# Kernel optimization log

Hardware: AMD Instinct MI355X
Metric: run time of the kernel (lower is better)

The kernel has to match this reference:

```python
import jax, jax.numpy as jnp
import numpy as np

NUM_HEADS = 16
LN_EPS = 1e-05


def setup_inputs() -> dict:
    key = jax.random.key(0)
    ks = jax.random.split(key, 10)
    B, S, H = 2, 2048, 1024
    s = 1.0 / np.sqrt(H)
    return {
        "hidden_states": jax.random.normal(ks[0], (B, S, H), dtype=jnp.float32),
        "Wq": jax.random.normal(ks[1], (H, H), dtype=jnp.float32) * s,
        "bq": jax.random.normal(ks[2], (H,), dtype=jnp.float32) * 0.02,
        "Wk": jax.random.normal(ks[3], (H, H), dtype=jnp.float32) * s,
        "bk": jax.random.normal(ks[4], (H,), dtype=jnp.float32) * 0.02,
        "Wv": jax.random.normal(ks[5], (H, H), dtype=jnp.float32) * s,
        "bv": jax.random.normal(ks[6], (H,), dtype=jnp.float32) * 0.02,
        "Wd": jax.random.normal(ks[7], (H, H), dtype=jnp.float32) * s,
        "bd": jax.random.normal(ks[8], (H,), dtype=jnp.float32) * 0.02,
        "ln_gamma": jnp.ones((H,), dtype=jnp.float32),
        "ln_beta": jnp.zeros((H,), dtype=jnp.float32),
    }


def reference(hidden_states, Wq, bq, Wk, bk, Wv, bv, Wd, bd, ln_gamma, ln_beta):
    B, S, H = hidden_states.shape
    nh = NUM_HEADS
    hd = H // nh

    # QKV projections (torch Linear: x @ W.T + b), split heads -> [B, nh, S, hd]
    def proj(W, b):
        y = jnp.einsum('bsh,oh->bso', hidden_states, W) + b
        return y.reshape(B, S, nh, hd).transpose(0, 2, 1, 3)

    q = proj(Wq, bq)
    k = proj(Wk, bk)
    v = proj(Wv, bv)

    # scaled dot-product attention: [B, nh, S, S]
    scores = jnp.einsum('bhqd,bhkd->bhqk', q, k) / jnp.sqrt(jnp.float32(hd))
    probs = jax.nn.softmax(scores, axis=-1)
    ctx = jnp.einsum('bhqk,bhkd->bhqd', probs, v)  # [B, nh, S, hd]
    ctx = ctx.transpose(0, 2, 1, 3).reshape(B, S, H)

    # output dense + residual + LayerNorm
    attn_out = jnp.einsum('bsh,oh->bso', ctx, Wd) + bd
    x = attn_out + hidden_states
    mu = jnp.mean(x, axis=-1, keepdims=True)
    var = jnp.mean(jnp.square(x - mu), axis=-1, keepdims=True)
    return (x - mu) * jax.lax.rsqrt(var + LN_EPS) * ln_gamma + ln_beta
```

## Files before the change

kernel.cpp:

```cpp
#include <hip/hip_runtime.h>

constexpr int kH    = 1024;
constexpr int kSEQ  = 2048;
constexpr int kBATCH= 2;
constexpr int kNH   = 16;
constexpr int kHD   = 64;
constexpr int kM    = 4096;

typedef _Float16 h8  __attribute__((ext_vector_type(8)));
typedef _Float16 h4  __attribute__((ext_vector_type(4)));
typedef float   f32x4 __attribute__((ext_vector_type(4)));

static __device__ __forceinline__ f32x4 mfma16(h8 a, h8 b, f32x4 c) {
  return __builtin_amdgcn_mfma_f32_16x16x32_f16(a, b, c, 0, 0, 0);
}

static __device__ __forceinline__ void gll16(const _Float16* g, _Float16* l) {
  __builtin_amdgcn_global_load_lds(
      (const __attribute__((address_space(1))) void*)g,
      (__attribute__((address_space(3))) void*)l, 16, 0, 0);
}

#define QSCALE 0.18033688011112042f
#define C0INIT (-5.770780163555854f)

__global__ __launch_bounds__(256) void cvt_all(
    const float* __restrict__ X,  const float* __restrict__ Wq,
    const float* __restrict__ Wk, const float* __restrict__ Wv,
    const float* __restrict__ Wd,
    _Float16* __restrict__ Xh,  _Float16* __restrict__ Wqh,
    _Float16* __restrict__ Wkh, _Float16* __restrict__ Wvh,
    _Float16* __restrict__ Wdh)
{
  int i = blockIdx.x * 256 + threadIdx.x;
  const float* src; _Float16* dst; int off;
  if (i < (kM * kH) / 4) {
    src = X; dst = Xh; off = i;
  } else {
    int j = i - (kM * kH) / 4;
    int w = j >> 18;
    off = j & 262143;
    src = (w == 0) ? Wq : (w == 1) ? Wk : (w == 2) ? Wv : Wd;
    dst = (w == 0) ? Wqh : (w == 1) ? Wkh : (w == 2) ? Wvh : Wdh;
  }
  float4 v = reinterpret_cast<const float4*>(src)[off];
  h4 o;
  o[0] = (_Float16)v.x; o[1] = (_Float16)v.y;
  o[2] = (_Float16)v.z; o[3] = (_Float16)v.w;
  reinterpret_cast<h4*>(dst)[off] = o;
}

__global__ __launch_bounds__(256, 2) void qkv_gemm(
    const _Float16* __restrict__ Xh,
    const _Float16* __restrict__ Wq, const _Float16* __restrict__ Wk,
    const _Float16* __restrict__ Wv,
    const float* __restrict__ bq, const float* __restrict__ bk,
    const float* __restrict__ bv,
    _Float16* __restrict__ Qo, _Float16* __restrict__ Ko, _Float16* __restrict__ Vo)
{
  const int proj = blockIdx.z;
  const _Float16* W   = (proj == 0) ? Wq : ((proj == 1) ? Wk : Wv);
  const float*    bias= (proj == 0) ? bq : ((proj == 1) ? bk : bv);
  _Float16*       Out = (proj == 0) ? Qo : ((proj == 1) ? Ko : Vo);

  const int m0 = blockIdx.y * 128, n0 = blockIdx.x * 128;
  __shared__ __align__(16) _Float16 As[2][128 * 32];
  __shared__ __align__(16) _Float16 Bs[2][128 * 32];

  const int tid  = threadIdx.x;
  const int wave = tid >> 6, lane = tid & 63, quad = lane >> 4, l16 = lane & 15;
  const int mw = (wave & 1) * 64, nw = (wave >> 1) * 64;

  f32x4 acc[4][4] = {};
  const int grow = wave * 32 + (lane >> 2);
  const int gcol = (lane & 3) * 8;
  const _Float16* Ag = Xh + (size_t)(m0 + grow) * kH + gcol;
  const _Float16* Bg = W  + (size_t)(n0 + grow) * kH + gcol;

  {
    gll16(Ag,            &As[0][wave * 1024]);
    gll16(Ag + 16 * kH,  &As[0][wave * 1024 + 512]);
    gll16(Bg,            &Bs[0][wave * 1024]);
    gll16(Bg + 16 * kH,  &Bs[0][wave * 1024 + 512]);
  }

  for (int k = 0; k < 32; ++k) {
    const int cur = k & 1;
    __syncthreads();
    if (k < 31) {
      const int k0 = (k + 1) * 32, nb = cur ^ 1;
      gll16(Ag + k0,           &As[nb][wave * 1024]);
      gll16(Ag + 16 * kH + k0, &As[nb][wave * 1024 + 512]);
      gll16(Bg + k0,           &Bs[nb][wave * 1024]);
      gll16(Bg + 16 * kH + k0, &Bs[nb][wave * 1024 + 512]);
    }
    h8 af[4], bf[4];
    #pragma unroll
    for (int mi = 0; mi < 4; ++mi)
      af[mi] = *reinterpret_cast<const h8*>(&As[cur][(mw + mi * 16 + l16) * 32 + quad * 8]);
    #pragma unroll
    for (int ni = 0; ni < 4; ++ni)
      bf[ni] = *reinterpret_cast<const h8*>(&Bs[cur][(nw + ni * 16 + l16) * 32 + quad * 8]);
    #pragma unroll
    for (int mi = 0; mi < 4; ++mi)
      #pragma unroll
      for (int ni = 0; ni < 4; ++ni)
        acc[mi][ni] = mfma16(af[mi], bf[ni], acc[mi][ni]);
  }

  #pragma unroll
  for (int mi = 0; mi < 4; ++mi)
  #pragma unroll
  for (int ni = 0; ni < 4; ++ni) {
    const int ng = n0 + nw + ni * 16 + l16;
    const float bv_ = bias[ng];
    const int hh = ng >> 6, dd = ng & 63;
    #pragma unroll
    for (int r = 0; r < 4; ++r) {
      const int mg = m0 + mw + mi * 16 + quad * 4 + r;
      float val = acc[mi][ni][r] + bv_;
      if (proj == 0) val *= QSCALE;
      const int bb = mg >> 11, srow = mg & 2047;
      Out[(((size_t)(bb * kNH + hh) * kSEQ) + srow) * kHD + dd] = (_Float16)val;
    }
  }
}

__global__ __launch_bounds__(256) void vtrans(const _Float16* __restrict__ V,
                                              _Float16* __restrict__ Vt)
{
  const int st = blockIdx.x;
  const int bh = blockIdx.y;
  __shared__ __align__(16) _Float16 Lt[64][72];
  const int t = threadIdx.x, r = t >> 2, c = (t & 3) * 16;
  const _Float16* src = V + (size_t)bh * kSEQ * kHD + (size_t)(st * 64 + r) * kHD + c;
  h8 p0 = *reinterpret_cast<const h8*>(src);
  h8 p1 = *reinterpret_cast<const h8*>(src + 8);
  #pragma unroll
  for (int e = 0; e < 8; ++e) Lt[c + e][r] = p0[e];
  #pragma unroll
  for (int e = 0; e < 8; ++e) Lt[c + 8 + e][r] = p1[e];
  __syncthreads();
  _Float16* dst = Vt + (size_t)bh * kHD * kSEQ + (size_t)r * kSEQ + st * 64 + c;
  *reinterpret_cast<h8*>(dst)     = *reinterpret_cast<const h8*>(&Lt[r][c]);
  *reinterpret_cast<h8*>(dst + 8) = *reinterpret_cast<const h8*>(&Lt[r][c + 8]);
}

__global__ __launch_bounds__(256, 3) void attn_kernel(
    const _Float16* __restrict__ Q, const _Float16* __restrict__ K,
    const _Float16* __restrict__ Vt, _Float16* __restrict__ Ctx)
{
  const int qt = blockIdx.x, bh = blockIdx.y;
  const int tid = threadIdx.x;
  const int wave = tid >> 6, lane = tid & 63, quad = lane >> 4, l16 = lane & 15;
  const int sw = l16 & 7;

  __shared__ __align__(16) _Float16 Kl[2][64 * 64];
  __shared__ __align__(16) _Float16 Vl[2][64 * 64];
  __shared__ __align__(16) _Float16 Pl[4][32 * 64];

  const _Float16* Qb = Q  + (size_t)bh * kSEQ * kHD;
  const _Float16* Kb = K  + (size_t)bh * kSEQ * kHD;
  const _Float16* Vb = Vt + (size_t)bh * kHD * kSEQ;

  const int qbase = qt * 128 + wave * 32;
  h8 qf[2][2];
  #pragma unroll
  for (int qh = 0; qh < 2; ++qh)
    #pragma unroll
    for (int dh = 0; dh < 2; ++dh)
      qf[qh][dh] = *reinterpret_cast<const h8*>(
          &Qb[(size_t)(qbase + qh * 16 + l16) * kHD + dh * 32 + quad * 8]);

  const int srow0  = lane >> 3;
  const int schunk = (lane & 7) ^ srow0;
  const int krow   = wave * 16 + srow0;
  const _Float16* Kg = Kb + (size_t)krow * kHD + schunk * 8;
  const _Float16* Vg = Vb + (size_t)krow * kSEQ + schunk * 8;
  _Float16* PlW = Pl[wave];

  float l_acc0 = 0.f, l_acc1 = 0.f;
  f32x4 o[2][4] = {};

  {
    gll16(Kg,                 &Kl[0][(wave * 16) * 64]);
    gll16(Kg + 8 * kHD,       &Kl[0][(wave * 16 + 8) * 64]);
    gll16(Vg,                 &Vl[0][(wave * 16) * 64]);
    gll16(Vg + 8 * kSEQ,      &Vl[0][(wave * 16 + 8) * 64]);
  }

  for (int kt = 0; kt < kSEQ / 64; ++kt) {
    const int cur = kt & 1;
    __syncthreads();
    if (kt + 1 < kSEQ / 64) {
      const int nb = cur ^ 1;
      const size_t ko = (size_t)(kt + 1) * 64;
      gll16(Kg + ko * kHD,             &Kl[nb][(wave * 16) * 64]);
      gll16(Kg + (ko + 8) * kHD,       &Kl[nb][(wave * 16 + 8) * 64]);
      gll16(Vg + ko,                   &Vl[nb][(wave * 16) * 64]);
      gll16(Vg + 8 * kSEQ + ko,        &Vl[nb][(wave * 16 + 8) * 64]);
    }
    const _Float16* Kc = Kl[cur];
    const _Float16* Vc = Vl[cur];

    f32x4 s[4][2];
    #pragma unroll
    for (int nt = 0; nt < 4; ++nt) {
      const int keyl = nt * 16 + l16;
      h8 ka0 = *reinterpret_cast<const h8*>(&Kc[keyl * 64 + ((quad     ) ^ sw) * 8]);
      h8 ka1 = *reinterpret_cast<const h8*>(&Kc[keyl * 64 + ((quad ^ 4) ^ sw) * 8]);
      #pragma unroll
      for (int qh = 0; qh < 2; ++qh) {
        f32x4 a = {C0INIT, C0INIT, C0INIT, C0INIT};
        a = mfma16(ka0, qf[qh][0], a);
        a = mfma16(ka1, qf[qh][1], a);
        s[nt][qh] = a;
      }
    }
    #pragma unroll
    for (int nt = 0; nt < 4; ++nt)
      #pragma unroll
      for (int qh = 0; qh < 2; ++qh) {
        float e0 = exp2f(s[nt][qh][0]);
        float e1 = exp2f(s[nt][qh][1]);
        float e2 = exp2f(s[nt][qh][2]);
        float e3 = exp2f(s[nt][qh][3]);
        float t4 = (e0 + e1) + (e2 + e3);
        if (qh == 0) l_acc0 += t4; else l_acc1 += t4;
        h4 pp;
        pp[0] = (_Float16)e0; pp[1] = (_Float16)e1;
        pp[2] = (_Float16)e2; pp[3] = (_Float16)e3;
        const int c8 = (nt * 2 + (quad >> 1)) ^ sw;
        *reinterpret_cast<h4*>(&PlW[(qh * 16 + l16) * 64 + c8 * 8 + (quad & 1) * 4]) = pp;
      }
    #pragma unroll
    for (int kc = 0; kc < 2; ++kc) {
      const int cs = ((kc * 4 + quad) ^ sw) * 8;
      h8 pa0 = *reinterpret_cast<const h8*>(&PlW[l16 * 64 + cs]);
      h8 pa1 = *reinterpret_cast<const h8*>(&PlW[(16 + l16) * 64 + cs]);
      #pragma unroll
      for (int dt = 0; dt < 4; ++dt) {
        h8 vbf = *reinterpret_cast<const h8*>(&Vc[(dt * 16 + l16) * 64 + cs]);
        o[0][dt] = mfma16(pa0, vbf, o[0][dt]);
        o[1][dt] = mfma16(pa1, vbf, o[1][dt]);
      }
    }
  }

  float li[2] = {l_acc0, l_acc1};
  #pragma unroll
  for (int qh = 0; qh < 2; ++qh) {
    li[qh] += __shfl_xor(li[qh], 16);
    li[qh] += __shfl_xor(li[qh], 32);
    li[qh] = 1.f / li[qh];
  }
  const int b = bh >> 4, hh = bh & 15;
  #pragma unroll
  for (int qh = 0; qh < 2; ++qh)
    #pragma unroll
    for (int r = 0; r < 4; ++r) {
      const float linv = __shfl(li[qh], quad * 4 + r);
      const int srow = qbase + qh * 16 + quad * 4 + r;
      #pragma unroll
      for (int dt = 0; dt < 4; ++dt) {
        const int col = hh * kHD + dt * 16 + l16;
        Ctx[((size_t)(b * kSEQ + srow)) * kH + col] =
            (_Float16)(o[qh][dt][r] * linv);
      }
    }
}

__global__ __launch_bounds__(256, 2) void dense_gemm(
    const _Float16* __restrict__ A, const _Float16* __restrict__ W,
    const float* __restrict__ bias, const float* __restrict__ resid,
    float* __restrict__ Out)
{
  const int m0 = blockIdx.y * 128, n0 = blockIdx.x * 128;
  __shared__ __align__(16) _Float16 As[2][128 * 32];
  __shared__ __align__(16) _Float16 Bs[2][128 * 32];
  const int tid  = threadIdx.x;
  const int wave = tid >> 6, lane = tid & 63, quad = lane >> 4, l16 = lane & 15;
  const int mw = (wave & 1) * 64, nw = (wave >> 1) * 64;
  f32x4 acc[4][4] = {};
  const int grow = wave * 32 + (lane >> 2);
  const int gcol = (lane & 3) * 8;
  const _Float16* Ag = A + (size_t)(m0 + grow) * kH + gcol;
  const _Float16* Bg = W + (size_t)(n0 + grow) * kH + gcol;

  {
    gll16(Ag,           &As[0][wave * 1024]);
    gll16(Ag + 16 * kH, &As[0][wave * 1024 + 512]);
    gll16(Bg,           &Bs[0][wave * 1024]);
    gll16(Bg + 16 * kH, &Bs[0][wave * 1024 + 512]);
  }

  for (int k = 0; k < 32; ++k) {
    const int cur = k & 1;
    __syncthreads();
    if (k < 31) {
      const int k0 = (k + 1) * 32, nb = cur ^ 1;
      gll16(Ag + k0,           &As[nb][wave * 1024]);
      gll16(Ag + 16 * kH + k0, &As[nb][wave * 1024 + 512]);
      gll16(Bg + k0,           &Bs[nb][wave * 1024]);
      gll16(Bg + 16 * kH + k0, &Bs[nb][wave * 1024 + 512]);
    }
    h8 af[4], bf[4];
    #pragma unroll
    for (int mi = 0; mi < 4; ++mi)
      af[mi] = *reinterpret_cast<const h8*>(&As[cur][(mw + mi * 16 + l16) * 32 + quad * 8]);
    #pragma unroll
    for (int ni = 0; ni < 4; ++ni)
      bf[ni] = *reinterpret_cast<const h8*>(&Bs[cur][(nw + ni * 16 + l16) * 32 + quad * 8]);
    #pragma unroll
    for (int mi = 0; mi < 4; ++mi)
      #pragma unroll
      for (int ni = 0; ni < 4; ++ni)
        acc[mi][ni] = mfma16(af[mi], bf[ni], acc[mi][ni]);
  }
  #pragma unroll
  for (int mi = 0; mi < 4; ++mi)
  #pragma unroll
  for (int ni = 0; ni < 4; ++ni) {
    const int ng = n0 + nw + ni * 16 + l16;
    const float bv_ = bias[ng];
    #pragma unroll
    for (int r = 0; r < 4; ++r) {
      const int mg = m0 + mw + mi * 16 + quad * 4 + r;
      Out[(size_t)mg * kH + ng] = acc[mi][ni][r] + bv_ + resid[(size_t)mg * kH + ng];
    }
  }
}

__global__ __launch_bounds__(256) void ln_kernel(const float* __restrict__ Tmp,
    const float* __restrict__ gamma, const float* __restrict__ beta,
    float* __restrict__ out)
{
  const int row = blockIdx.x;
  const float4 v = reinterpret_cast<const float4*>(Tmp + (size_t)row * kH)[threadIdx.x];
  float s  = v.x + v.y + v.z + v.w;
  float ss = v.x * v.x + v.y * v.y + v.z * v.z + v.w * v.w;
  #pragma unroll
  for (int off = 32; off > 0; off >>= 1) {
    s  += __shfl_down(s, off);
    ss += __shfl_down(ss, off);
  }
  __shared__ float red[8];
  const int wave = threadIdx.x >> 6, lane = threadIdx.x & 63;
  if (lane == 0) { red[wave] = s; red[4 + wave] = ss; }
  __syncthreads();
  s  = red[0] + red[1] + red[2] + red[3];
  ss = red[4] + red[5] + red[6] + red[7];
  const float mu   = s * (1.f / kH);
  const float var  = ss * (1.f / kH) - mu * mu;
  const float rstd = rsqrtf(var + 1e-5f);
  const float4 g  = reinterpret_cast<const float4*>(gamma)[threadIdx.x];
  const float4 bb = reinterpret_cast<const float4*>(beta)[threadIdx.x];
  float4 o;
  o.x = (v.x - mu) * rstd * g.x + bb.x;
  o.y = (v.y - mu) * rstd * g.y + bb.y;
  o.z = (v.z - mu) * rstd * g.z + bb.z;
  o.w = (v.w - mu) * rstd * g.w + bb.w;
  reinterpret_cast<float4*>(out + (size_t)row * kH)[threadIdx.x] = o;
}

extern "C" void kernel_launch(void* const* d_in, const int* in_sizes, int n_in,
                              void* d_out, int out_size, void* d_ws, size_t ws_size,
                              hipStream_t stream) {
  const float* hs    = (const float*)d_in[0];
  const float* Wq    = (const float*)d_in[1];
  const float* bq    = (const float*)d_in[2];
  const float* Wk    = (const float*)d_in[3];
  const float* bk    = (const float*)d_in[4];
  const float* Wv    = (const float*)d_in[5];
  const float* bv    = (const float*)d_in[6];
  const float* Wd    = (const float*)d_in[7];
  const float* bd    = (const float*)d_in[8];
  const float* gamma = (const float*)d_in[9];
  const float* beta  = (const float*)d_in[10];
  float* out = (float*)d_out;

  char* ws = (char*)d_ws;
  _Float16* Xh  = (_Float16*)(ws + 0);
  _Float16* Wqh = (_Float16*)(ws + 8388608);
  _Float16* Wkh = (_Float16*)(ws + 10485760);
  _Float16* Wvh = (_Float16*)(ws + 12582912);
  _Float16* Wdh = (_Float16*)(ws + 14680064);
  _Float16* Qh  = (_Float16*)(ws + 16777216);
  _Float16* Kh  = (_Float16*)(ws + 25165824);
  _Float16* Vh  = (_Float16*)(ws + 33554432);
  _Float16* Ch  = (_Float16*)(ws + 41943040);
  _Float16* Vtb = Xh;
  float*    Tmp = (float*)Qh;

  cvt_all<<<8192, 256, 0, stream>>>(hs, Wq, Wk, Wv, Wd, Xh, Wqh, Wkh, Wvh, Wdh);
  qkv_gemm<<<dim3(kH / 128, kM / 128, 3), 256, 0, stream>>>(
      Xh, Wqh, Wkh, Wvh, bq, bk, bv, Qh, Kh, Vh);
  vtrans<<<dim3(kSEQ / 64, kBATCH * kNH), 256, 0, stream>>>(Vh, Vtb);
  attn_kernel<<<dim3(kSEQ / 128, kBATCH * kNH), 256, 0, stream>>>(Qh, Kh, Vtb, Ch);
  dense_gemm<<<dim3(kH / 128, kM / 128), 256, 0, stream>>>(Ch, Wdh, bd, hs, Tmp);
  ln_kernel<<<kM, 256, 0, stream>>>(Tmp, gamma, beta, out);
}
```

Before: 231.3 us.

## Split attention over key ranges with a merge kernel and MFMA row sums

Attention now splits the key dimension into four chunks across a third grid axis and uses 128-thread blocks where each wave covers 64 query rows with 32-key tiles. Each split writes unnormalized fp16 partial outputs and fp32 row sums, and a new merge kernel adds them and normalizes into the context buffer. Row sums are computed with an MFMA against a ones vector rather than scalar adds, and the workspace is remapped. The aim is more blocks for better CU occupancy and a lower per-tile cost, at the price of extra partial-result traffic, one more launch, and fp16 rounding of the partial sums.

```diff
diff --git a/kernel.cpp b/kernel.cpp
--- a/kernel.cpp
+++ b/kernel.cpp
@@ -6,6 +6,8 @@
 constexpr int kNH   = 16;
 constexpr int kHD   = 64;
 constexpr int kM    = 4096;
+constexpr int kSPLIT= 4;
+constexpr int kKEYS = kSEQ / kSPLIT;
 
 typedef _Float16 h8  __attribute__((ext_vector_type(8)));
 typedef _Float16 h4  __attribute__((ext_vector_type(4)));
@@ -146,128 +148,137 @@
   *reinterpret_cast<h8*>(dst + 8) = *reinterpret_cast<const h8*>(&Lt[r][c + 8]);
 }
 
-__global__ __launch_bounds__(256, 3) void attn_kernel(
+__global__ __launch_bounds__(128, 3) void attn_kernel(
     const _Float16* __restrict__ Q, const _Float16* __restrict__ K,
-    const _Float16* __restrict__ Vt, _Float16* __restrict__ Ctx)
-{
-  const int qt = blockIdx.x, bh = blockIdx.y;
+    const _Float16* __restrict__ Vt, _Float16* __restrict__ Op,
+    float* __restrict__ lp)
+{
+  const int qt = blockIdx.x, bh = blockIdx.y, split = blockIdx.z;
   const int tid = threadIdx.x;
   const int wave = tid >> 6, lane = tid & 63, quad = lane >> 4, l16 = lane & 15;
-  const int sw = l16 & 7;
-
-  __shared__ __align__(16) _Float16 Kl[2][64 * 64];
-  __shared__ __align__(16) _Float16 Vl[2][64 * 64];
-  __shared__ __align__(16) _Float16 Pl[4][32 * 64];
+  const int sw3 = l16 & 3, sw7 = l16 & 7;
+
+  __shared__ __align__(16) _Float16 Kl[2][32 * 64];
+  __shared__ __align__(16) _Float16 Vl[2][64 * 32];
+  __shared__ __align__(16) _Float16 Pl[2][64 * 32];
 
   const _Float16* Qb = Q  + (size_t)bh * kSEQ * kHD;
   const _Float16* Kb = K  + (size_t)bh * kSEQ * kHD;
   const _Float16* Vb = Vt + (size_t)bh * kHD * kSEQ;
-
-  const int qbase = qt * 128 + wave * 32;
-  h8 qf[2][2];
-  #pragma unroll
-  for (int qh = 0; qh < 2; ++qh)
+  const int soff = split * kKEYS;
+
+  const int qbase = qt * 128 + wave * 64;
+  h8 qf[4][2];
+  #pragma unroll
+  for (int qh = 0; qh < 4; ++qh)
     #pragma unroll
     for (int dh = 0; dh < 2; ++dh)
       qf[qh][dh] = *reinterpret_cast<const h8*>(
           &Qb[(size_t)(qbase + qh * 16 + l16) * kHD + dh * 32 + quad * 8]);
 
-  const int srow0  = lane >> 3;
-  const int schunk = (lane & 7) ^ srow0;
-  const int krow   = wave * 16 + srow0;
-  const _Float16* Kg = Kb + (size_t)krow * kHD + schunk * 8;
-  const _Float16* Vg = Vb + (size_t)krow * kSEQ + schunk * 8;
+  const int krw = lane >> 3;
+  const int kch = (lane & 7) ^ krw;
+  const _Float16* Kg = Kb + (size_t)(soff + wave * 16 + krw) * kHD + kch * 8;
+  const int vdl = lane >> 2;
+  const int vch = (lane & 3) ^ (vdl & 3);
+  const _Float16* Vg = Vb + (size_t)(wave * 32 + vdl) * kSEQ + soff + vch * 8;
   _Float16* PlW = Pl[wave];
 
-  float l_acc0 = 0.f, l_acc1 = 0.f;
-  f32x4 o[2][4] = {};
-
-  {
-    gll16(Kg,                 &Kl[0][(wave * 16) * 64]);
-    gll16(Kg + 8 * kHD,       &Kl[0][(wave * 16 + 8) * 64]);
-    gll16(Vg,                 &Vl[0][(wave * 16) * 64]);
-    gll16(Vg + 8 * kSEQ,      &Vl[0][(wave * 16 + 8) * 64]);
-  }
-
-  for (int kt = 0; kt < kSEQ / 64; ++kt) {
+  f32x4 o[4][4] = {};
+  f32x4 ol[4] = {};
+  h8 vones = {(_Float16)1.f, (_Float16)1.f, (_Float16)1.f, (_Float16)1.f,
+              (_Float16)1.f, (_Float16)1.f, (_Float16)1.f, (_Float16)1.f};
+
+  gll16(Kg,               &Kl[0][(wave * 16) * 64]);
+  gll16(Kg + 8 * kHD,     &Kl[0][(wave * 16 + 8) * 64]);
+  gll16(Vg,               &Vl[0][(wave * 32) * 32]);
+  gll16(Vg + 16 * kSEQ,   &Vl[0][(wave * 32 + 16) * 32]);
+
+  for (int kt = 0; kt < kKEYS / 32; ++kt) {
     const int cur = kt & 1;
     __syncthreads();
-    if (kt + 1 < kSEQ / 64) {
+    if (kt + 1 < kKEYS / 32) {
       const int nb = cur ^ 1;
-      const size_t ko = (size_t)(kt + 1) * 64;
-      gll16(Kg + ko * kHD,             &Kl[nb][(wave * 16) * 64]);
-      gll16(Kg + (ko + 8) * kHD,       &Kl[nb][(wave * 16 + 8) * 64]);
-      gll16(Vg + ko,                   &Vl[nb][(wave * 16) * 64]);
-      gll16(Vg + 8 * kSEQ + ko,        &Vl[nb][(wave * 16 + 8) * 64]);
+      const int ko = (kt + 1) * 32;
+      gll16(Kg + (size_t)ko * kHD,            &Kl[nb][(wave * 16) * 64]);
+      gll16(Kg + (size_t)(ko + 8) * kHD,      &Kl[nb][(wave * 16 + 8) * 64]);
+      gll16(Vg + ko,                          &Vl[nb][(wave * 32) * 32]);
+      gll16(Vg + 16 * kSEQ + ko,              &Vl[nb][(wave * 32 + 16) * 32]);
     }
     const _Float16* Kc = Kl[cur];
     const _Float16* Vc = Vl[cur];
 
-    f32x4 s[4][2];
-    #pragma unroll
-    for (int nt = 0; nt < 4; ++nt) {
+    #pragma unroll
+    for (int nt = 0; nt < 2; ++nt) {
       const int keyl = nt * 16 + l16;
-      h8 ka0 = *reinterpret_cast<const h8*>(&Kc[keyl * 64 + ((quad     ) ^ sw) * 8]);
-      h8 ka1 = *reinterpret_cast<const h8*>(&Kc[keyl * 64 + ((quad ^ 4) ^ sw) * 8]);
+      h8 ka0 = *reinterpret_cast<const h8*>(&Kc[keyl * 64 + ((quad     ) ^ sw7) * 8]);
+      h8 ka1 = *reinterpret_cast<const h8*>(&Kc[keyl * 64 + ((quad ^ 4) ^ sw7) * 8]);
       #pragma unroll
-      for (int qh = 0; qh < 2; ++qh) {
+      for (int qh = 0; qh < 4; ++qh) {
         f32x4 a = {C0INIT, C0INIT, C0INIT, C0INIT};
         a = mfma16(ka0, qf[qh][0], a);
         a = mfma16(ka1, qf[qh][1], a);
-        s[nt][qh] = a;
+        h4 pp;
+        pp[0] = (_Float16)exp2f(a[0]); pp[1] = (_Float16)exp2f(a[1]);
+        pp[2] = (_Float16)exp2f(a[2]); pp[3] = (_Float16)exp2f(a[3]);
+        const int row = qh * 16 + l16;
+        const int c = (nt * 2 + (quad >> 1)) ^ sw3;
+        *reinterpret_cast<h4*>(&PlW[row * 32 + c * 8 + (quad & 1) * 4]) = pp;
       }
     }
-    #pragma unroll
-    for (int nt = 0; nt < 4; ++nt)
+    h8 pa[4];
+    #pragma unroll
+    for (int qh = 0; qh < 4; ++qh)
+      pa[qh] = *reinterpret_cast<const h8*>(
+          &PlW[(qh * 16 + l16) * 32 + (quad ^ sw3) * 8]);
+    #pragma unroll
+    for (int dt = 0; dt < 4; ++dt) {
+      h8 vb = *reinterpret_cast<const h8*>(
+          &Vc[(dt * 16 + l16) * 32 + (quad ^ sw3) * 8]);
       #pragma unroll
-      for (int qh = 0; qh < 2; ++qh) {
-        float e0 = exp2f(s[nt][qh][0]);
-        float e1 = exp2f(s[nt][qh][1]);
-        float e2 = exp2f(s[nt][qh][2]);
-        float e3 = exp2f(s[nt][qh][3]);
-        float t4 = (e0 + e1) + (e2 + e3);
-        if (qh == 0) l_acc0 += t4; else l_acc1 += t4;
-        h4 pp;
-        pp[0] = (_Float16)e0; pp[1] = (_Float16)e1;
-        pp[2] = (_Float16)e2; pp[3] = (_Float16)e3;
-        const int c8 = (nt * 2 + (quad >> 1)) ^ sw;
-        *reinterpret_cast<h4*>(&PlW[(qh * 16 + l16) * 64 + c8 * 8 + (quad & 1) * 4]) = pp;
-      }
-    #pragma unroll
-    for (int kc = 0; kc < 2; ++kc) {
-      const int cs = ((kc * 4 + quad) ^ sw) * 8;
-      h8 pa0 = *reinterpret_cast<const h8*>(&PlW[l16 * 64 + cs]);
-      h8 pa1 = *reinterpret_cast<const h8*>(&PlW[(16 + l16) * 64 + cs]);
+      for (int qh = 0; qh < 4; ++qh)
+        o[qh][dt] = mfma16(pa[qh], vb, o[qh][dt]);
+    }
+    #pragma unroll
+    for (int qh = 0; qh < 4; ++qh)
+      ol[qh] = mfma16(pa[qh], vones, ol[qh]);
+  }
+
+  const size_t pbase = ((size_t)(split * (kBATCH * kNH) + bh)) * kSEQ;
+  #pragma unroll
+  for (int qh = 0; qh < 4; ++qh)
+    #pragma unroll
+    for (int r = 0; r < 4; ++r) {
+      const int qrow = qbase + qh * 16 + quad * 4 + r;
+      if (l16 == 0) lp[pbase + qrow] = ol[qh][r];
       #pragma unroll
-      for (int dt = 0; dt < 4; ++dt) {
-        h8 vbf = *reinterpret_cast<const h8*>(&Vc[(dt * 16 + l16) * 64 + cs]);
-        o[0][dt] = mfma16(pa0, vbf, o[0][dt]);
-        o[1][dt] = mfma16(pa1, vbf, o[1][dt]);
-      }
-    }
-  }
-
-  float li[2] = {l_acc0, l_acc1};
-  #pragma unroll
-  for (int qh = 0; qh < 2; ++qh) {
-    li[qh] += __shfl_xor(li[qh], 16);
-    li[qh] += __shfl_xor(li[qh], 32);
-    li[qh] = 1.f / li[qh];
-  }
+      for (int dt = 0; dt < 4; ++dt)
+        Op[(pbase + qrow) * kHD + dt * 16 + l16] = (_Float16)o[qh][dt][r];
+    }
+}
+
+__global__ __launch_bounds__(256) void attn_merge(
+    const _Float16* __restrict__ Op, const float* __restrict__ lp,
+    _Float16* __restrict__ Ctx)
+{
+  const int t = blockIdx.x * 256 + threadIdx.x;
+  const int d8 = t & 7, q = (t >> 3) & (kSEQ - 1), bh = t >> 14;
+  float acc[8] = {};
+  float l = 0.f;
+  #pragma unroll
+  for (int s = 0; s < kSPLIT; ++s) {
+    const size_t pbase = ((size_t)(s * (kBATCH * kNH) + bh)) * kSEQ + q;
+    h8 v = *reinterpret_cast<const h8*>(&Op[pbase * kHD + d8 * 8]);
+    #pragma unroll
+    for (int e = 0; e < 8; ++e) acc[e] += (float)v[e];
+    l += lp[pbase];
+  }
+  const float inv = 1.f / l;
   const int b = bh >> 4, hh = bh & 15;
-  #pragma unroll
-  for (int qh = 0; qh < 2; ++qh)
-    #pragma unroll
-    for (int r = 0; r < 4; ++r) {
-      const float linv = __shfl(li[qh], quad * 4 + r);
-      const int srow = qbase + qh * 16 + quad * 4 + r;
-      #pragma unroll
-      for (int dt = 0; dt < 4; ++dt) {
-        const int col = hh * kHD + dt * 16 + l16;
-        Ctx[((size_t)(b * kSEQ + srow)) * kH + col] =
-            (_Float16)(o[qh][dt][r] * linv);
-      }
-    }
+  h8 ov;
+  #pragma unroll
+  for (int e = 0; e < 8; ++e) ov[e] = (_Float16)(acc[e] * inv);
+  *reinterpret_cast<h8*>(&Ctx[((size_t)(b * kSEQ + q)) * kH + hh * kHD + d8 * 8]) = ov;
 }
 
 __global__ __launch_bounds__(256, 2) void dense_gemm(
@@ -380,23 +391,27 @@
   float* out = (float*)d_out;
 
   char* ws = (char*)d_ws;
-  _Float16* Xh  = (_Float16*)(ws + 0);
-  _Float16* Wqh = (_Float16*)(ws + 8388608);
-  _Float16* Wkh = (_Float16*)(ws + 10485760);
-  _Float16* Wvh = (_Float16*)(ws + 12582912);
-  _Float16* Wdh = (_Float16*)(ws + 14680064);
-  _Float16* Qh  = (_Float16*)(ws + 16777216);
-  _Float16* Kh  = (_Float16*)(ws + 25165824);
-  _Float16* Vh  = (_Float16*)(ws + 33554432);
-  _Float16* Ch  = (_Float16*)(ws + 41943040);
-  _Float16* Vtb = Xh;
-  float*    Tmp = (float*)Qh;
+  _Float16* Xh   = (_Float16*)(ws + 0);
+  _Float16* Wqh  = (_Float16*)(ws + 8388608);
+  _Float16* Wkh  = (_Float16*)(ws + 10485760);
+  _Float16* Wvh  = (_Float16*)(ws + 12582912);
+  _Float16* Wdh  = (_Float16*)(ws + 14680064);
+  _Float16* Qh   = (_Float16*)(ws + 16777216);
+  _Float16* Kh   = (_Float16*)(ws + 25165824);
+  _Float16* Vh   = (_Float16*)(ws + 33554432);
+  _Float16* Vtb  = Xh;
+  float*    lpart= (float*)Wqh;
+  _Float16* Opart= (_Float16*)(ws + 33554432);
+  _Float16* Ctx  = Qh;
+  float*    Tmp  = (float*)(ws + 50331648);
 
   cvt_all<<<8192, 256, 0, stream>>>(hs, Wq, Wk, Wv, Wd, Xh, Wqh, Wkh, Wvh, Wdh);
   qkv_gemm<<<dim3(kH / 128, kM / 128, 3), 256, 0, stream>>>(
       Xh, Wqh, Wkh, Wvh, bq, bk, bv, Qh, Kh, Vh);
   vtrans<<<dim3(kSEQ / 64, kBATCH * kNH), 256, 0, stream>>>(Vh, Vtb);
-  attn_kernel<<<dim3(kSEQ / 128, kBATCH * kNH), 256, 0, stream>>>(Qh, Kh, Vtb, Ch);
-  dense_gemm<<<dim3(kH / 128, kM / 128), 256, 0, stream>>>(Ch, Wdh, bd, hs, Tmp);
+  attn_kernel<<<dim3(kSEQ / 128, kBATCH * kNH, kSPLIT), 128, 0, stream>>>(
+      Qh, Kh, Vtb, Opart, lpart);
+  attn_merge<<<2048, 256, 0, stream>>>(Opart, lpart, Ctx);
+  dense_gemm<<<dim3(kH / 128, kM / 128), 256, 0, stream>>>(Ctx, Wdh, bd, hs, Tmp);
   ln_kernel<<<kM, 256, 0, stream>>>(Tmp, gamma, beta, out);
 }
```

After: 243.8 us. 1.05x slower.
